# Kernel tuning notes

Measured on AMD Instinct MI355X. Metric: run time of the kernel, lower is better.

Reference implementation:

```python
import jax, jax.numpy as jnp
import numpy as np

B = 256
N = 1024
K = 64
BASIS = 8
SINKHORN_ITERS = 1
TEMP = 0.2
EPS = 1e-5


def log_sinkhorn(log_alpha, n_iters=SINKHORN_ITERS, temperature=TEMP):
    la = log_alpha / temperature
    for _ in range(n_iters):
        la = la - jax.scipy.special.logsumexp(la, axis=-1, keepdims=True)
        la = la - jax.scipy.special.logsumexp(la, axis=-2, keepdims=True)
    return jnp.exp(la)


def setup_inputs() -> dict:
    key = jax.random.key(0)
    k1, k2, k3, k4 = jax.random.split(key, 4)
    x = jax.random.normal(k1, (B, N * K), dtype=jnp.float32)
    A_logits = 0.01 * jax.random.normal(k2, (N, N), dtype=jnp.float32)
    W_1 = 0.01 * jax.random.normal(k3, (N, BASIS), dtype=jnp.float32)
    W_V = 0.01 * jax.random.normal(k4, (BASIS, K, K), dtype=jnp.float32)
    gamma2 = jnp.ones((N,), dtype=jnp.float32)  # LayerNorm(N) weight
    beta2 = jnp.zeros((N,), dtype=jnp.float32)  # LayerNorm(N) bias
    return {"x": x, "A_logits": A_logits, "W_1": W_1, "W_V": W_V,
            "gamma2": gamma2, "beta2": beta2}


def layernorm(x, gamma, beta):
    mu = jnp.mean(x, axis=-1, keepdims=True)
    var = jnp.mean(jnp.square(x - mu), axis=-1, keepdims=True)
    return (x - mu) * jax.lax.rsqrt(var + EPS) * gamma + beta


def reference(x, A_logits, W_1, W_V, gamma2, beta2):
    x_reshaped = x.reshape(B, N, K)
    A = log_sinkhorn(A_logits)                       # [N, N] doubly-stochastic
    W_logits = jnp.einsum('tk,kde->tde', W_1, W_V)   # [N, K, K]
    W = log_sinkhorn(W_logits)                       # per-block doubly-stochastic
    x_local = jnp.einsum('bni,nio->bno', x_reshaped, W)  # N independent KxK GEMMs
    x_local = layernorm(jnp.transpose(x_local, (0, 2, 1)), gamma2, beta2)  # [B,K,N]
    x_global = x_local @ A                           # [B,K,N]
    x_global = jnp.transpose(x_global, (0, 2, 1))    # [B,N,K]
    return x_global.reshape(B, N * K)
```

## Files before the change

### kernel.cpp

```cpp
#include <hip/hip_runtime.h>
#include <hip/hip_fp16.h>
#include <math.h>

#define NDIM 1024
#define KDIM 64
#define BDIM 256
#define BKDIM 16384

typedef unsigned short u16;
typedef __attribute__((ext_vector_type(8))) short bf16x8;
typedef __attribute__((ext_vector_type(4))) float f32x4;

__device__ __forceinline__ float bf2f(u16 u) {
  union { unsigned u; float f; } x; x.u = ((unsigned)u) << 16; return x.f;
}
__device__ __forceinline__ u16 f2bf(float f) {
  union { float f; unsigned u; } x; x.f = f;
  unsigned u = x.u;
  u += 0x7fffu + ((u >> 16) & 1u);
  return (u16)(u >> 16);
}
__device__ __forceinline__ u16 f2h(float f) { return __half_as_ushort(__float2half(f)); }
__device__ __forceinline__ float h2f(u16 u) { return __half2float(__ushort_as_half(u)); }

__device__ __forceinline__ void async16(const u16* g, u16* s) {
  __builtin_amdgcn_global_load_lds(
      (const __attribute__((address_space(1))) unsigned int*)g,
      (__attribute__((address_space(3))) unsigned int*)s,
      16, 0, 0);
}

__global__ __launch_bounds__(256) void k_row_lse(const float* __restrict__ Alog,
                                                 float* __restrict__ r) {
  int m = blockIdx.x, t = threadIdx.x;
  float v[4], mx = -3.0e38f;
#pragma unroll
  for (int j = 0; j < 4; j++) {
    v[j] = Alog[m * NDIM + t + j * 256] * 5.0f;
    mx = fmaxf(mx, v[j]);
  }
  __shared__ float sred[256];
  sred[t] = mx; __syncthreads();
  for (int s = 128; s > 0; s >>= 1) { if (t < s) sred[t] = fmaxf(sred[t], sred[t + s]); __syncthreads(); }
  float bm = sred[0]; __syncthreads();
  float sm = 0.f;
#pragma unroll
  for (int j = 0; j < 4; j++) sm += expf(v[j] - bm);
  sred[t] = sm; __syncthreads();
  for (int s = 128; s > 0; s >>= 1) { if (t < s) sred[t] += sred[t + s]; __syncthreads(); }
  if (t == 0) r[m] = bm + logf(sred[0]);
}

__global__ __launch_bounds__(256) void k_col_dt(const float* __restrict__ Alog,
                                                const float* __restrict__ r,
                                                u16* __restrict__ Dt) {
  int n = blockIdx.x, t = threadIdx.x;
  float v[4], mx = -3.0e38f;
#pragma unroll
  for (int j = 0; j < 4; j++) {
    int m = t + j * 256;
    v[j] = Alog[m * NDIM + n] * 5.0f - r[m];
    mx = fmaxf(mx, v[j]);
  }
  __shared__ float sred[256];
  sred[t] = mx; __syncthreads();
  for (int s = 128; s > 0; s >>= 1) { if (t < s) sred[t] = fmaxf(sred[t], sred[t + s]); __syncthreads(); }
  float bm = sred[0]; __syncthreads();
  float sm = 0.f;
#pragma unroll
  for (int j = 0; j < 4; j++) sm += expf(v[j] - bm);
  sred[t] = sm; __syncthreads();
  for (int s = 128; s > 0; s >>= 1) { if (t < s) sred[t] += sred[t + s]; __syncthreads(); }
  float cn = bm + logf(sred[0]);
#pragma unroll
  for (int j = 0; j < 4; j++) {
    int m = t + j * 256;
    Dt[n * NDIM + m] = f2bf(expf(v[j] - cn) - 0.0009765625f);
  }
}

__global__ __launch_bounds__(256) void k_w(const float* __restrict__ W1,
                                           const float* __restrict__ WV,
                                           u16* __restrict__ Wt) {
  int tb = blockIdx.x, t = threadIdx.x;
  int d = t >> 2, q = t & 3;
  float w1[8];
#pragma unroll
  for (int k = 0; k < 8; k++) w1[k] = W1[tb * 8 + k];
  float la[16];
#pragma unroll
  for (int j = 0; j < 16; j++) la[j] = 0.f;
#pragma unroll
  for (int k = 0; k < 8; k++) {
    float wk = w1[k];
    const float4* base = (const float4*)&WV[k * 4096 + d * 64 + q * 16];
#pragma unroll
    for (int v = 0; v < 4; v++) {
      float4 f = base[v];
      la[v * 4 + 0] += wk * f.x; la[v * 4 + 1] += wk * f.y;
      la[v * 4 + 2] += wk * f.z; la[v * 4 + 3] += wk * f.w;
    }
  }
  float mx = -3.0e38f;
#pragma unroll
  for (int j = 0; j < 16; j++) { la[j] *= 5.0f; mx = fmaxf(mx, la[j]); }
  float sm = 0.f;
#pragma unroll
  for (int j = 0; j < 16; j++) sm += expf(la[j] - mx);
  for (int off = 1; off < 4; off <<= 1) {
    float mo = __shfl_xor(mx, off), so = __shfl_xor(sm, off);
    float mn = fmaxf(mx, mo);
    sm = sm * expf(mx - mn) + so * expf(mo - mn);
    mx = mn;
  }
  float rl = mx + logf(sm);
  __shared__ float sla[64 * 65];
#pragma unroll
  for (int j = 0; j < 16; j++) sla[d * 65 + q * 16 + j] = la[j] - rl;
  __syncthreads();
  int e = t >> 2, jj = t & 3;
  float lb[16]; float m2 = -3.0e38f;
#pragma unroll
  for (int i = 0; i < 16; i++) { lb[i] = sla[(jj * 16 + i) * 65 + e]; m2 = fmaxf(m2, lb[i]); }
  float s2 = 0.f;
#pragma unroll
  for (int i = 0; i < 16; i++) s2 += expf(lb[i] - m2);
  for (int off = 1; off < 4; off <<= 1) {
    float mo = __shfl_xor(m2, off), so = __shfl_xor(s2, off);
    float mn = fmaxf(m2, mo);
    s2 = s2 * expf(m2 - mn) + so * expf(mo - mn);
    m2 = mn;
  }
  float cl = m2 + logf(s2);
#pragma unroll
  for (int i = 0; i < 16; i++)
    Wt[tb * 4096 + e * 64 + jj * 16 + i] = f2bf(expf(lb[i] - cl));
}

__global__ __launch_bounds__(256) void k_gemm1(const float* __restrict__ x,
                                               const u16* __restrict__ Wt,
                                               u16* __restrict__ xl) {
  __shared__ __align__(16) u16 xhi[128 * 64];
  __shared__ __align__(16) u16 xlo[128 * 64];
  __shared__ __align__(16) u16 wsm[64 * 64];
  int n = blockIdx.x, t = threadIdx.x;
  {
    const uint4* src = (const uint4*)(Wt + n * 4096);
    uint4* dst = (uint4*)wsm;
    dst[t] = src[t];
    dst[t + 256] = src[t + 256];
  }
  int w = t >> 6, l = t & 63, q = l >> 4, lr = l & 15;
  int col4 = (t & 15) * 4;
  int rbase = t >> 4;
  for (int half = 0; half < 2; half++) {
    int b0 = half * 128;
    __syncthreads();
#pragma unroll
    for (int j = 0; j < 8; j++) {
      int rl2 = j * 16 + rbase;
      float4 v = *(const float4*)&x[(size_t)(b0 + rl2) * 65536 + n * 64 + col4];
      ushort4 hi, lo;
      hi.x = f2bf(v.x); lo.x = f2bf(v.x - bf2f(hi.x));
      hi.y = f2bf(v.y); lo.y = f2bf(v.y - bf2f(hi.y));
      hi.z = f2bf(v.z); lo.z = f2bf(v.z - bf2f(hi.z));
      hi.w = f2bf(v.w); lo.w = f2bf(v.w - bf2f(hi.w));
      *(ushort4*)&xhi[rl2 * 64 + col4] = hi;
      *(ushort4*)&xlo[rl2 * 64 + col4] = lo;
    }
    __syncthreads();
    f32x4 acc[2][4] = {};
#pragma unroll
    for (int ks = 0; ks < 2; ks++) {
      bf16x8 ah[2], al[2], bfr[4];
#pragma unroll
      for (int mi = 0; mi < 2; mi++) {
        ah[mi] = *(const bf16x8*)&xhi[(w * 32 + mi * 16 + lr) * 64 + ks * 32 + q * 8];
        al[mi] = *(const bf16x8*)&xlo[(w * 32 + mi * 16 + lr) * 64 + ks * 32 + q * 8];
      }
#pragma unroll
      for (int ni = 0; ni < 4; ni++)
        bfr[ni] = *(const bf16x8*)&wsm[(ni * 16 + lr) * 64 + ks * 32 + q * 8];
#pragma unroll
      for (int mi = 0; mi < 2; mi++)
#pragma unroll
        for (int ni = 0; ni < 4; ni++) {
          acc[mi][ni] = __builtin_amdgcn_mfma_f32_16x16x32_bf16(ah[mi], bfr[ni], acc[mi][ni], 0, 0, 0);
          acc[mi][ni] = __builtin_amdgcn_mfma_f32_16x16x32_bf16(al[mi], bfr[ni], acc[mi][ni], 0, 0, 0);
        }
    }
#pragma unroll
    for (int mi = 0; mi < 2; mi++)
#pragma unroll
      for (int ni = 0; ni < 4; ni++) {
        int o = ni * 16 + lr;
#pragma unroll
        for (int reg = 0; reg < 4; reg++) {
          int b = b0 + w * 32 + mi * 16 + q * 4 + reg;
          xl[n * BKDIM + b * 64 + o] = f2h(acc[mi][ni][reg]);
        }
      }
  }
}

__global__ __launch_bounds__(256) void k_ln(const u16* __restrict__ xl,
                                            const float* __restrict__ g2,
                                            const float* __restrict__ b2,
                                            u16* __restrict__ xln,
                                            float* __restrict__ sON) {
  __shared__ float s_sum[32 * 64], s_ssq[32 * 64], s_wsx[32 * 64];
  __shared__ float s_gs[32], s_bs[32];
  __shared__ float s_mu[64], s_al[64];
  __shared__ __align__(16) u16 ldsT[64 * 136];
  int blk = blockIdx.x, t = threadIdx.x;
  int c0 = blk * 64;
  int rg = t >> 3, cs = t & 7;
  float sum[8], ssq[8], wsx[8];
#pragma unroll
  for (int j = 0; j < 8; j++) { sum[j] = 0.f; ssq[j] = 0.f; wsx[j] = 0.f; }
  float gs = 0.f, bs = 0.f;
  for (int it = 0; it < 32; it++) {
    int row = it * 32 + rg;
    bf16x8 v = *(const bf16x8*)&xl[row * BKDIM + c0 + cs * 8];
    float gm = g2[row], bt = b2[row];
    gs += gm; bs += bt;
#pragma unroll
    for (int j = 0; j < 8; j++) {
      float f = h2f((u16)v[j]);
      sum[j] += f; ssq[j] += f * f; wsx[j] += f * gm;
    }
  }
#pragma unroll
  for (int j = 0; j < 8; j++) {
    s_sum[rg * 64 + cs * 8 + j] = sum[j];
    s_ssq[rg * 64 + cs * 8 + j] = ssq[j];
    s_wsx[rg * 64 + cs * 8 + j] = wsx[j];
  }
  if (cs == 0) { s_gs[rg] = gs; s_bs[rg] = bs; }
  __syncthreads();
  if (t < 64) {
    float S = 0.f, Q = 0.f, Wx = 0.f, G = 0.f, Bt = 0.f;
    for (int k = 0; k < 32; k++) {
      S += s_sum[k * 64 + t]; Q += s_ssq[k * 64 + t]; Wx += s_wsx[k * 64 + t];
      G += s_gs[k]; Bt += s_bs[k];
    }
    float mu = S * (1.0f / 1024.0f);
    float var = Q * (1.0f / 1024.0f) - mu * mu;
    float al = rsqrtf(var + 1e-5f);
    s_mu[t] = mu; s_al[t] = al;
    sON[c0 + t] = (al * (Wx - mu * G) + Bt) * (1.0f / 1024.0f);
  }
  __syncthreads();
  for (int ch = 0; ch < 8; ch++) {
#pragma unroll
    for (int si = 0; si < 4; si++) {
      int rl = si * 32 + rg;
      int row = ch * 128 + rl;
      bf16x8 v = *(const bf16x8*)&xl[row * BKDIM + c0 + cs * 8];
      float gm = g2[row], bt = b2[row];
#pragma unroll
      for (int j = 0; j < 8; j++) {
        int col = cs * 8 + j;
        float f = (h2f((u16)v[j]) - s_mu[col]) * s_al[col] * gm + bt;
        ldsT[col * 136 + rl] = f2bf(f);
      }
    }
    __syncthreads();
    int c2 = t >> 2, sg = t & 3;
    const u16* src = &ldsT[c2 * 136 + sg * 32];
    u16* dst = &xln[(c0 + c2) * NDIM + ch * 128 + sg * 32];
#pragma unroll
    for (int k = 0; k < 4; k++)
      *(bf16x8*)&dst[k * 8] = *(const bf16x8*)&src[k * 8];
    __syncthreads();
  }
}

__global__ __launch_bounds__(256) void k_gemm2(const u16* __restrict__ Dt,
                                               const u16* __restrict__ xln,
                                               const float* __restrict__ sON,
                                               float* __restrict__ out) {
  __shared__ __align__(16) u16 lA[128 * 64];
  __shared__ __align__(16) u16 lB[128 * 64];
  int bkt = blockIdx.x, n2t = blockIdx.y;
  int t = threadIdx.x, w = t >> 6, l = t & 63;
  int q = l >> 4, lr = l & 15;
  int rr = l >> 3;
  int cc = (l & 7) ^ rr;
  const u16* gA = Dt  + (size_t)(n2t * 128) * NDIM + cc * 8;
  const u16* gB = xln + (size_t)(bkt * 128) * NDIM + cc * 8;
  f32x4 acc[4][4] = {};
  for (int kt = 0; kt < 16; kt++) {
#pragma unroll
    for (int j = 0; j < 4; j++) {
      int ci = j * 4 + w;
      int row = ci * 8 + rr;
      async16(gA + (size_t)row * NDIM + kt * 64, &lA[ci * 512 + l * 8]);
      async16(gB + (size_t)row * NDIM + kt * 64, &lB[ci * 512 + l * 8]);
    }
    __syncthreads();
#pragma unroll
    for (int ks = 0; ks < 2; ks++) {
      int pc = ((ks * 4 + q) ^ (lr & 7)) * 8;
      bf16x8 af[4], bfr[4];
#pragma unroll
      for (int mi = 0; mi < 4; mi++)
        af[mi] = *(const bf16x8*)&lA[((w >> 1) * 64 + mi * 16 + lr) * 64 + pc];
#pragma unroll
      for (int ni = 0; ni < 4; ni++)
        bfr[ni] = *(const bf16x8*)&lB[((w & 1) * 64 + ni * 16 + lr) * 64 + pc];
#pragma unroll
      for (int mi = 0; mi < 4; mi++)
#pragma unroll
        for (int ni = 0; ni < 4; ni++)
          acc[mi][ni] = __builtin_amdgcn_mfma_f32_16x16x32_bf16(af[mi], bfr[ni], acc[mi][ni], 0, 0, 0);
    }
    __syncthreads();
  }
#pragma unroll
  for (int ni = 0; ni < 4; ni++) {
    int bk = bkt * 128 + (w & 1) * 64 + ni * 16 + lr;
    float sN = sON[bk];
    int b = bk >> 6, o = bk & 63;
#pragma unroll
    for (int mi = 0; mi < 4; mi++)
#pragma unroll
      for (int reg = 0; reg < 4; reg++) {
        int n2 = n2t * 128 + (w >> 1) * 64 + mi * 16 + q * 4 + reg;
        out[(size_t)b * 65536 + n2 * 64 + o] = acc[mi][ni][reg] + sN;
      }
  }
}

extern "C" void kernel_launch(void* const* d_in, const int* in_sizes, int n_in,
                              void* d_out, int out_size, void* d_ws, size_t ws_size,
                              hipStream_t stream) {
  const float* x    = (const float*)d_in[0];
  const float* Alog = (const float*)d_in[1];
  const float* W1   = (const float*)d_in[2];
  const float* WV   = (const float*)d_in[3];
  const float* g2   = (const float*)d_in[4];
  const float* b2   = (const float*)d_in[5];
  float* out = (float*)d_out;
  char* ws = (char*)d_ws;

  u16*   xln = (u16*)(ws);
  u16*   Wt  = (u16*)(ws + 33554432ull);
  u16*   Dt  = (u16*)(ws + 41943040ull);
  float* r   = (float*)(ws + 44040192ull);
  float* sON = (float*)(ws + 44044288ull);
  u16*   xl  = (u16*)((char*)d_out + 33554432ull);

  k_row_lse<<<dim3(1024), dim3(256), 0, stream>>>(Alog, r);
  k_col_dt<<<dim3(1024), dim3(256), 0, stream>>>(Alog, r, Dt);
  k_w<<<dim3(1024), dim3(256), 0, stream>>>(W1, WV, Wt);
  k_gemm1<<<dim3(1024), dim3(256), 0, stream>>>(x, Wt, xl);
  k_ln<<<dim3(256), dim3(256), 0, stream>>>(xl, g2, b2, xln, sON);
  k_gemm2<<<dim3(128, 8), dim3(256), 0, stream>>>(Dt, xln, sON, out);
}
```

Measured before the change: 231.8 us.

## Split LayerNorm into parallel stat/finalize/apply kernels and simplify gemm1

Replaces the single 256-block LayerNorm kernel with three kernels: a 1024-block partial-statistics pass, a small finalize pass and a 1024-block normalize-and-transpose pass using an XOR-swizzled LDS tile. The goal is more parallelism for the LN stage, which was limited by its small grid. gemm1 now loads x straight from global memory into MFMA fragments, with no LDS staging or barriers. Sinkhorn kernels switch to the fast __expf/__logf intrinsics. The price is two extra launches, partial sums written to scratch in the output buffer, and slightly less accurate exp/log.

```diff
diff --git a/kernel.cpp b/kernel.cpp
--- a/kernel.cpp
+++ b/kernel.cpp
@@ -45,10 +45,10 @@
   float bm = sred[0]; __syncthreads();
   float sm = 0.f;
 #pragma unroll
-  for (int j = 0; j < 4; j++) sm += expf(v[j] - bm);
+  for (int j = 0; j < 4; j++) sm += __expf(v[j] - bm);
   sred[t] = sm; __syncthreads();
   for (int s = 128; s > 0; s >>= 1) { if (t < s) sred[t] += sred[t + s]; __syncthreads(); }
-  if (t == 0) r[m] = bm + logf(sred[0]);
+  if (t == 0) r[m] = bm + __logf(sred[0]);
 }
 
 __global__ __launch_bounds__(256) void k_col_dt(const float* __restrict__ Alog,
@@ -68,14 +68,14 @@
   float bm = sred[0]; __syncthreads();
   float sm = 0.f;
 #pragma unroll
-  for (int j = 0; j < 4; j++) sm += expf(v[j] - bm);
+  for (int j = 0; j < 4; j++) sm += __expf(v[j] - bm);
   sred[t] = sm; __syncthreads();
   for (int s = 128; s > 0; s >>= 1) { if (t < s) sred[t] += sred[t + s]; __syncthreads(); }
-  float cn = bm + logf(sred[0]);
+  float cn = bm + __logf(sred[0]);
 #pragma unroll
   for (int j = 0; j < 4; j++) {
     int m = t + j * 256;
-    Dt[n * NDIM + m] = f2bf(expf(v[j] - cn) - 0.0009765625f);
+    Dt[n * NDIM + m] = f2bf(__expf(v[j] - cn) - 0.0009765625f);
   }
 }
 
@@ -106,14 +106,14 @@
   for (int j = 0; j < 16; j++) { la[j] *= 5.0f; mx = fmaxf(mx, la[j]); }
   float sm = 0.f;
 #pragma unroll
-  for (int j = 0; j < 16; j++) sm += expf(la[j] - mx);
+  for (int j = 0; j < 16; j++) sm += __expf(la[j] - mx);
   for (int off = 1; off < 4; off <<= 1) {
     float mo = __shfl_xor(mx, off), so = __shfl_xor(sm, off);
     float mn = fmaxf(mx, mo);
-    sm = sm * expf(mx - mn) + so * expf(mo - mn);
+    sm = sm * __expf(mx - mn) + so * __expf(mo - mn);
     mx = mn;
   }
-  float rl = mx + logf(sm);
+  float rl = mx + __logf(sm);
   __shared__ float sla[64 * 65];
 #pragma unroll
   for (int j = 0; j < 16; j++) sla[d * 65 + q * 16 + j] = la[j] - rl;
@@ -124,155 +124,172 @@
   for (int i = 0; i < 16; i++) { lb[i] = sla[(jj * 16 + i) * 65 + e]; m2 = fmaxf(m2, lb[i]); }
   float s2 = 0.f;
 #pragma unroll
-  for (int i = 0; i < 16; i++) s2 += expf(lb[i] - m2);
+  for (int i = 0; i < 16; i++) s2 += __expf(lb[i] - m2);
   for (int off = 1; off < 4; off <<= 1) {
     float mo = __shfl_xor(m2, off), so = __shfl_xor(s2, off);
     float mn = fmaxf(m2, mo);
-    s2 = s2 * expf(m2 - mn) + so * expf(mo - mn);
+    s2 = s2 * __expf(m2 - mn) + so * __expf(mo - mn);
     m2 = mn;
   }
-  float cl = m2 + logf(s2);
+  float cl = m2 + __logf(s2);
 #pragma unroll
   for (int i = 0; i < 16; i++)
-    Wt[tb * 4096 + e * 64 + jj * 16 + i] = f2bf(expf(lb[i] - cl));
+    Wt[tb * 4096 + e * 64 + jj * 16 + i] = f2bf(__expf(lb[i] - cl));
 }
 
 __global__ __launch_bounds__(256) void k_gemm1(const float* __restrict__ x,
                                                const u16* __restrict__ Wt,
                                                u16* __restrict__ xl) {
-  __shared__ __align__(16) u16 xhi[128 * 64];
-  __shared__ __align__(16) u16 xlo[128 * 64];
-  __shared__ __align__(16) u16 wsm[64 * 64];
-  int n = blockIdx.x, t = threadIdx.x;
-  {
-    const uint4* src = (const uint4*)(Wt + n * 4096);
-    uint4* dst = (uint4*)wsm;
-    dst[t] = src[t];
-    dst[t + 256] = src[t + 256];
-  }
-  int w = t >> 6, l = t & 63, q = l >> 4, lr = l & 15;
-  int col4 = (t & 15) * 4;
-  int rbase = t >> 4;
-  for (int half = 0; half < 2; half++) {
-    int b0 = half * 128;
-    __syncthreads();
-#pragma unroll
-    for (int j = 0; j < 8; j++) {
-      int rl2 = j * 16 + rbase;
-      float4 v = *(const float4*)&x[(size_t)(b0 + rl2) * 65536 + n * 64 + col4];
-      ushort4 hi, lo;
-      hi.x = f2bf(v.x); lo.x = f2bf(v.x - bf2f(hi.x));
-      hi.y = f2bf(v.y); lo.y = f2bf(v.y - bf2f(hi.y));
-      hi.z = f2bf(v.z); lo.z = f2bf(v.z - bf2f(hi.z));
-      hi.w = f2bf(v.w); lo.w = f2bf(v.w - bf2f(hi.w));
-      *(ushort4*)&xhi[rl2 * 64 + col4] = hi;
-      *(ushort4*)&xlo[rl2 * 64 + col4] = lo;
-    }
-    __syncthreads();
-    f32x4 acc[2][4] = {};
-#pragma unroll
-    for (int ks = 0; ks < 2; ks++) {
-      bf16x8 ah[2], al[2], bfr[4];
-#pragma unroll
-      for (int mi = 0; mi < 2; mi++) {
-        ah[mi] = *(const bf16x8*)&xhi[(w * 32 + mi * 16 + lr) * 64 + ks * 32 + q * 8];
-        al[mi] = *(const bf16x8*)&xlo[(w * 32 + mi * 16 + lr) * 64 + ks * 32 + q * 8];
+  int n = blockIdx.x, t = threadIdx.x, w = t >> 6, l = t & 63;
+  int q = l >> 4, lr = l & 15;
+  const float* xb = x + n * 64;
+  const u16* wb = Wt + n * 4096;
+  f32x4 acc[4][4] = {};
+#pragma unroll
+  for (int ks = 0; ks < 2; ks++) {
+    bf16x8 bfr[4];
+#pragma unroll
+    for (int ni = 0; ni < 4; ni++)
+      bfr[ni] = *(const bf16x8*)&wb[(ni * 16 + lr) * 64 + ks * 32 + q * 8];
+#pragma unroll
+    for (int mi = 0; mi < 4; mi++) {
+      int b = w * 64 + mi * 16 + lr;
+      const float* xr = xb + (size_t)b * 65536 + ks * 32 + q * 8;
+      float4 v0 = *(const float4*)xr;
+      float4 v1 = *(const float4*)(xr + 4);
+      float vf[8] = {v0.x, v0.y, v0.z, v0.w, v1.x, v1.y, v1.z, v1.w};
+      bf16x8 ah, al;
+#pragma unroll
+      for (int j = 0; j < 8; j++) {
+        u16 h = f2bf(vf[j]);
+        ah[j] = (short)h;
+        al[j] = (short)f2bf(vf[j] - bf2f(h));
       }
 #pragma unroll
-      for (int ni = 0; ni < 4; ni++)
-        bfr[ni] = *(const bf16x8*)&wsm[(ni * 16 + lr) * 64 + ks * 32 + q * 8];
-#pragma unroll
-      for (int mi = 0; mi < 2; mi++)
-#pragma unroll
-        for (int ni = 0; ni < 4; ni++) {
-          acc[mi][ni] = __builtin_amdgcn_mfma_f32_16x16x32_bf16(ah[mi], bfr[ni], acc[mi][ni], 0, 0, 0);
-          acc[mi][ni] = __builtin_amdgcn_mfma_f32_16x16x32_bf16(al[mi], bfr[ni], acc[mi][ni], 0, 0, 0);
-        }
-    }
-#pragma unroll
-    for (int mi = 0; mi < 2; mi++)
-#pragma unroll
       for (int ni = 0; ni < 4; ni++) {
-        int o = ni * 16 + lr;
-#pragma unroll
-        for (int reg = 0; reg < 4; reg++) {
-          int b = b0 + w * 32 + mi * 16 + q * 4 + reg;
-          xl[n * BKDIM + b * 64 + o] = f2h(acc[mi][ni][reg]);
-        }
+        acc[mi][ni] = __builtin_amdgcn_mfma_f32_16x16x32_bf16(ah, bfr[ni], acc[mi][ni], 0, 0, 0);
+        acc[mi][ni] = __builtin_amdgcn_mfma_f32_16x16x32_bf16(al, bfr[ni], acc[mi][ni], 0, 0, 0);
       }
-  }
-}
-
-__global__ __launch_bounds__(256) void k_ln(const u16* __restrict__ xl,
-                                            const float* __restrict__ g2,
-                                            const float* __restrict__ b2,
-                                            u16* __restrict__ xln,
-                                            float* __restrict__ sON) {
-  __shared__ float s_sum[32 * 64], s_ssq[32 * 64], s_wsx[32 * 64];
-  __shared__ float s_gs[32], s_bs[32];
-  __shared__ float s_mu[64], s_al[64];
-  __shared__ __align__(16) u16 ldsT[64 * 136];
-  int blk = blockIdx.x, t = threadIdx.x;
-  int c0 = blk * 64;
-  int rg = t >> 3, cs = t & 7;
-  float sum[8], ssq[8], wsx[8];
-#pragma unroll
-  for (int j = 0; j < 8; j++) { sum[j] = 0.f; ssq[j] = 0.f; wsx[j] = 0.f; }
-  float gs = 0.f, bs = 0.f;
-  for (int it = 0; it < 32; it++) {
-    int row = it * 32 + rg;
-    bf16x8 v = *(const bf16x8*)&xl[row * BKDIM + c0 + cs * 8];
-    float gm = g2[row], bt = b2[row];
-    gs += gm; bs += bt;
+    }
+  }
+#pragma unroll
+  for (int mi = 0; mi < 4; mi++)
+#pragma unroll
+    for (int ni = 0; ni < 4; ni++) {
+      int o = ni * 16 + lr;
+#pragma unroll
+      for (int reg = 0; reg < 4; reg++) {
+        int b = w * 64 + mi * 16 + q * 4 + reg;
+        xl[n * BKDIM + b * 64 + o] = f2h(acc[mi][ni][reg]);
+      }
+    }
+}
+
+__global__ __launch_bounds__(256) void k_stat(const u16* __restrict__ xl,
+                                              const float* __restrict__ g2,
+                                              float* __restrict__ Ps,
+                                              float* __restrict__ Pq,
+                                              float* __restrict__ Pw) {
+  __shared__ float sS[16 * 132], sQ[16 * 132], sW[16 * 132];
+  int cb = blockIdx.x, mc = blockIdx.y, t = threadIdx.x;
+  int c0 = cb * 128;
+  int rg = t >> 4, cs = (t & 15) * 8;
+  float sum[8], ssq[8], wg[8];
+#pragma unroll
+  for (int j = 0; j < 8; j++) { sum[j] = 0.f; ssq[j] = 0.f; wg[j] = 0.f; }
+  for (int it = 0; it < 8; it++) {
+    int row = mc * 128 + it * 16 + rg;
+    bf16x8 v = *(const bf16x8*)&xl[(size_t)row * BKDIM + c0 + cs];
+    float gm = g2[row];
 #pragma unroll
     for (int j = 0; j < 8; j++) {
       float f = h2f((u16)v[j]);
-      sum[j] += f; ssq[j] += f * f; wsx[j] += f * gm;
+      sum[j] += f; ssq[j] += f * f; wg[j] += f * gm;
     }
   }
 #pragma unroll
   for (int j = 0; j < 8; j++) {
-    s_sum[rg * 64 + cs * 8 + j] = sum[j];
-    s_ssq[rg * 64 + cs * 8 + j] = ssq[j];
-    s_wsx[rg * 64 + cs * 8 + j] = wsx[j];
-  }
-  if (cs == 0) { s_gs[rg] = gs; s_bs[rg] = bs; }
+    sS[rg * 132 + cs + j] = sum[j];
+    sQ[rg * 132 + cs + j] = ssq[j];
+    sW[rg * 132 + cs + j] = wg[j];
+  }
   __syncthreads();
-  if (t < 64) {
-    float S = 0.f, Q = 0.f, Wx = 0.f, G = 0.f, Bt = 0.f;
-    for (int k = 0; k < 32; k++) {
-      S += s_sum[k * 64 + t]; Q += s_ssq[k * 64 + t]; Wx += s_wsx[k * 64 + t];
-      G += s_gs[k]; Bt += s_bs[k];
-    }
-    float mu = S * (1.0f / 1024.0f);
-    float var = Q * (1.0f / 1024.0f) - mu * mu;
-    float al = rsqrtf(var + 1e-5f);
-    s_mu[t] = mu; s_al[t] = al;
-    sON[c0 + t] = (al * (Wx - mu * G) + Bt) * (1.0f / 1024.0f);
+  if (t < 128) {
+    float S = 0.f, Q = 0.f, W = 0.f;
+    for (int k = 0; k < 16; k++) {
+      S += sS[k * 132 + t]; Q += sQ[k * 132 + t]; W += sW[k * 132 + t];
+    }
+    Ps[mc * BKDIM + c0 + t] = S;
+    Pq[mc * BKDIM + c0 + t] = Q;
+    Pw[mc * BKDIM + c0 + t] = W;
+  }
+}
+
+__global__ __launch_bounds__(256) void k_fin(const float* __restrict__ Ps,
+                                             const float* __restrict__ Pq,
+                                             const float* __restrict__ Pw,
+                                             const float* __restrict__ g2,
+                                             const float* __restrict__ b2,
+                                             float* __restrict__ mu,
+                                             float* __restrict__ al,
+                                             float* __restrict__ sON) {
+  __shared__ float red[512];
+  int t = threadIdx.x;
+  float g = 0.f, b = 0.f;
+#pragma unroll
+  for (int k = 0; k < 4; k++) { g += g2[t * 4 + k]; b += b2[t * 4 + k]; }
+  red[t] = g; red[256 + t] = b; __syncthreads();
+  for (int s = 128; s > 0; s >>= 1) {
+    if (t < s) { red[t] += red[t + s]; red[256 + t] += red[256 + t + s]; }
+    __syncthreads();
+  }
+  float G = red[0], Bt = red[256];
+  int bk = blockIdx.x * 256 + t;
+  float S = 0.f, Q = 0.f, W = 0.f;
+#pragma unroll
+  for (int mc = 0; mc < 8; mc++) {
+    S += Ps[mc * BKDIM + bk]; Q += Pq[mc * BKDIM + bk]; W += Pw[mc * BKDIM + bk];
+  }
+  float m_ = S * (1.0f / 1024.0f);
+  float var = Q * (1.0f / 1024.0f) - m_ * m_;
+  float a = rsqrtf(var + 1e-5f);
+  mu[bk] = m_; al[bk] = a;
+  sON[bk] = (a * (W - m_ * G) + Bt) * (1.0f / 1024.0f);
+}
+
+__global__ __launch_bounds__(256) void k_apply(const u16* __restrict__ xl,
+                                               const float* __restrict__ g2,
+                                               const float* __restrict__ b2,
+                                               const float* __restrict__ mu,
+                                               const float* __restrict__ al,
+                                               u16* __restrict__ xln) {
+  __shared__ __align__(16) u16 ldsT[128 * 128];
+  int bkt = blockIdx.x, mc = blockIdx.y, t = threadIdx.x;
+  int c0 = bkt * 128;
+  int r = t >> 4, cs = t & 15;
+  float mu8[8], al8[8];
+#pragma unroll
+  for (int j = 0; j < 8; j++) { mu8[j] = mu[c0 + cs * 8 + j]; al8[j] = al[c0 + cs * 8 + j]; }
+  int key = cs << 3;
+  for (int it = 0; it < 8; it++) {
+    int m_ = it * 16 + r;
+    int row = mc * 128 + m_;
+    bf16x8 v = *(const bf16x8*)&xl[(size_t)row * BKDIM + c0 + cs * 8];
+    float gm = g2[row], bt = b2[row];
+    int pm = m_ ^ key;
+#pragma unroll
+    for (int j = 0; j < 8; j++) {
+      float f = (h2f((u16)v[j]) - mu8[j]) * al8[j] * gm + bt;
+      ldsT[(cs * 8 + j) * 128 + pm] = f2bf(f);
+    }
   }
   __syncthreads();
-  for (int ch = 0; ch < 8; ch++) {
-#pragma unroll
-    for (int si = 0; si < 4; si++) {
-      int rl = si * 32 + rg;
-      int row = ch * 128 + rl;
-      bf16x8 v = *(const bf16x8*)&xl[row * BKDIM + c0 + cs * 8];
-      float gm = g2[row], bt = b2[row];
-#pragma unroll
-      for (int j = 0; j < 8; j++) {
-        int col = cs * 8 + j;
-        float f = (h2f((u16)v[j]) - s_mu[col]) * s_al[col] * gm + bt;
-        ldsT[col * 136 + rl] = f2bf(f);
-      }
-    }
-    __syncthreads();
-    int c2 = t >> 2, sg = t & 3;
-    const u16* src = &ldsT[c2 * 136 + sg * 32];
-    u16* dst = &xln[(c0 + c2) * NDIM + ch * 128 + sg * 32];
-#pragma unroll
-    for (int k = 0; k < 4; k++)
-      *(bf16x8*)&dst[k * 8] = *(const bf16x8*)&src[k * 8];
-    __syncthreads();
+  int ms = (t & 15) * 8;
+  for (int it = 0; it < 8; it++) {
+    int col = it * 16 + (t >> 4);
+    int key2 = (col >> 3) << 3;
+    bf16x8 o = *(const bf16x8*)&ldsT[col * 128 + (ms ^ key2)];
+    *(bf16x8*)&xln[(size_t)(c0 + col) * NDIM + mc * 128 + ms] = o;
   }
 }
 
@@ -350,11 +367,18 @@
   float* r   = (float*)(ws + 44040192ull);
   float* sON = (float*)(ws + 44044288ull);
   u16*   xl  = (u16*)((char*)d_out + 33554432ull);
+  float* Ps  = (float*)((char*)d_out);
+  float* Pq  = (float*)((char*)d_out + 524288ull);
+  float* Pw  = (float*)((char*)d_out + 1048576ull);
+  float* mu  = (float*)((char*)d_out + 1572864ull);
+  float* al  = (float*)((char*)d_out + 1638400ull);
 
   k_row_lse<<<dim3(1024), dim3(256), 0, stream>>>(Alog, r);
   k_col_dt<<<dim3(1024), dim3(256), 0, stream>>>(Alog, r, Dt);
   k_w<<<dim3(1024), dim3(256), 0, stream>>>(W1, WV, Wt);
   k_gemm1<<<dim3(1024), dim3(256), 0, stream>>>(x, Wt, xl);
-  k_ln<<<dim3(256), dim3(256), 0, stream>>>(xl, g2, b2, xln, sON);
+  k_stat<<<dim3(128, 8), dim3(256), 0, stream>>>(xl, g2, Ps, Pq, Pw);
+  k_fin<<<dim3(64), dim3(256), 0, stream>>>(Ps, Pq, Pw, g2, b2, mu, al, sON);
+  k_apply<<<dim3(128, 8), dim3(256), 0, stream>>>(xl, g2, b2, mu, al, xln);
   k_gemm2<<<dim3(128, 8), dim3(256), 0, stream>>>(Dt, xln, sON, out);
 }
```

Result: no change. 229.9 us (-0.8%).
